# Performance work log

Hardware: AMD Instinct MI355X
Metric: run time of the kernel (lower is better)

The kernel has to match this reference:

```python
import jax, jax.numpy as jnp
import numpy as np

B, C, H, W = 4, 384, 56, 56
K, S = 5, 7


def setup_inputs() -> dict:
    key = jax.random.key(0)
    k1, k2, k3, k4, k5 = jax.random.split(key, 5)
    x = jax.random.normal(k1, (B, C, H, W), dtype=jnp.float32)
    ctx = jax.random.normal(k2, (B, C, H, W), dtype=jnp.float32)
    # 1x1 conv weights stored as (out_ch, in_ch) matrices
    Wq = jax.random.normal(k3, (C // 2, C), dtype=jnp.float32) * (1.0 / np.sqrt(C))
    Wk = jax.random.normal(k4, (C // 2, C), dtype=jnp.float32) * (1.0 / np.sqrt(C))
    Wwd = jax.random.normal(k5, (K * K, S * S), dtype=jnp.float32) * (1.0 / np.sqrt(S * S))
    return {"x": x, "ctx": ctx, "Wq": Wq, "Wk": Wk, "Wwd": Wwd}


def reference(x, ctx, Wq, Wk, Wwd):
    b, c, h, w = x.shape
    kk = K
    # q: 1x1 conv then flatten spatial -> (B, C/2, HW)
    q = jnp.einsum('dc,bchw->bdhw', Wq, x).reshape(b, c // 2, h * w)
    # adaptive avg pool to S x S (H,W multiples of S -> uniform 8x8 bins)
    ctx_p = ctx.reshape(b, c, S, h // S, S, w // S).mean(axis=(3, 5))  # (B,C,S,S)
    kf = jnp.einsum('dc,bcst->bdst', Wk, ctx_p).reshape(b, c // 2, S * S)
    # attention over region centers: (B, HW, S*S)
    A = jax.nn.softmax(jnp.einsum('bdn,bds->bns', q, kf), axis=-1)
    # dynamic per-pixel kernels via 1x1 conv S*S -> k*k: (B, k*k, H, W)
    dyn = jnp.einsum('js,bns->bjn', Wwd, A).reshape(b, kk * kk, h, w)
    # unfold x (im2col with padding k//2) -> (B, C, k*k, H, W)
    pad = kk // 2
    xp = jnp.pad(x, ((0, 0), (0, 0), (pad, pad), (pad, pad)))
    patches = jnp.stack(
        [xp[:, :, i:i + h, j:j + w] for i in range(kk) for j in range(kk)], axis=2
    )
    # per-pixel weighted reduction over the k*k taps
    out = jnp.einsum('bcjhw,bjhw->bchw', patches, dyn)
    return out
```

## Files before the change

### kernel.cpp

```cpp
#include <hip/hip_runtime.h>

#define BB 4
#define CCH 384
#define HH 56
#define WWD 56
#define HW 3136
#define S2 49
#define S2P 52
#define D2 192
#define K2 25
#define XSP 20
#define NBS 196

__global__ __launch_bounds__(256) void gtpool_k(const float* __restrict__ Wa,
                                                const float* __restrict__ Wb,
                                                const float* __restrict__ ctx,
                                                float* __restrict__ GT,
                                                float* __restrict__ PT) {
    __shared__ float sh[6144];
    int blk = blockIdx.x;
    int t = threadIdx.x;
    if (blk < 576) {
        float* As = sh;
        float* Bs = sh + 3072;
        int bi = blk % 24, bj = blk / 24;
        int tj = t & 15, ti = t >> 4;
#pragma unroll
        for (int k = 0; k < 3; k++) {
            int idx = t + 256 * k;
            int d = idx >> 2, q = idx & 3;
            *(float4*)&As[idx * 4] = *(const float4*)&Wa[(size_t)d * CCH + bi * 16 + 4 * q];
            *(float4*)&Bs[idx * 4] = *(const float4*)&Wb[(size_t)d * CCH + bj * 16 + 4 * q];
        }
        __syncthreads();
        float acc = 0.f;
#pragma unroll 8
        for (int d = 0; d < D2; d++)
            acc += As[d * 16 + ti] * Bs[d * 16 + tj];
        GT[(size_t)(bi * 16 + ti) * CCH + bj * 16 + tj] = acc;
    } else {
        float* part = sh;
        int pb = blk - 576;
        int b  = pb / 84;
        int rem = pb - b * 84;
        int sy = rem / 12;
        int cg = rem - sy * 12;
        int c0 = cg * 32;
        const float* base = ctx + ((size_t)(b * CCH + c0)) * HW + sy * 8 * WWD;
#pragma unroll
        for (int k = 0; k < 14; k++) {
            int g = t + 256 * k;
            int cc = g / 112;
            int r2 = g - cc * 112;
            float4 v = *(const float4*)(base + (size_t)cc * HW + 4 * r2);
            part[g] = (v.x + v.y) + (v.z + v.w);
        }
        __syncthreads();
        if (t < 224) {
            int cc = t / 7, sx = t - cc * 7;
            float sum = 0.f;
#pragma unroll
            for (int r = 0; r < 8; r++) {
                sum += part[cc * 112 + r * 14 + 2 * sx]
                     + part[cc * 112 + r * 14 + 2 * sx + 1];
            }
            int bs = b * S2 + sy * 7 + sx;
            PT[(size_t)(c0 + cc) * NBS + bs] = sum * (1.f / 64.f);
        }
    }
}

__global__ __launch_bounds__(256) void mv2_k(const float* __restrict__ GTt,
                                             const float* __restrict__ PT,
                                             float* __restrict__ M) {
    int t = threadIdx.x;
    int r = blockIdx.x * 2 + (t >> 7);
    int c = t & 127;
    bool has1 = (c < NBS - 128);
    int c1 = has1 ? c + 128 : c;
    const float* g = GTt + (size_t)r * CCH;
    float a0 = 0.f, a1 = 0.f;
#pragma unroll 8
    for (int i = 0; i < CCH; i++) {
        float gv = g[i];
        a0 += gv * PT[(size_t)i * NBS + c];
        a1 += gv * PT[(size_t)i * NBS + c1];
    }
    int b0 = c / S2, s0 = c - b0 * S2;
    M[((size_t)(b0 * CCH + r)) * S2P + s0] = a0;
    if (has1) {
        int bs1 = c + 128;
        int b1 = bs1 / S2, s1 = bs1 - b1 * S2;
        M[((size_t)(b1 * CCH + r)) * S2P + s1] = a1;
    }
    if (c >= 68 && c < 80) {
        int rem = c - 68;
        int bb = rem / 3, sp = 49 + rem % 3;
        M[((size_t)(bb * CCH + r)) * S2P + sp] = 0.f;
    }
}

__global__ __launch_bounds__(256) void attn_k(const float* __restrict__ x,
                                              const float* __restrict__ M,
                                              const float* __restrict__ Wwd,
                                              float* __restrict__ dyn) {
    __shared__ __align__(16) float smem[96 * XSP + 96 * S2P];
    __shared__ __align__(16) float sc[16 * S2P];
    __shared__ __align__(16) float wl[K2 * S2P];
    float* xs  = smem;
    float* Ms  = smem + 96 * XSP;
    float* red = smem;

    int b  = blockIdx.x / 196;
    int n0 = (blockIdx.x % 196) * 16;
    int t  = threadIdx.x;
    int pxg = t & 3, sg = (t >> 2) & 3, slice = t >> 4;

    float4 acc4[4][4];
#pragma unroll
    for (int k = 0; k < 4; k++)
#pragma unroll
        for (int j = 0; j < 4; j++) acc4[k][j] = make_float4(0.f, 0.f, 0.f, 0.f);

    const float* xb = x + (size_t)b * CCH * HW + n0;
    const float* Mb = M + (size_t)b * CCH * S2P;

#pragma unroll
    for (int k = 0; k < 5; k++) {
        int i = t + 256 * k;
        int j = i / S2P, ss = i - j * S2P;
        wl[i] = (ss < S2) ? Wwd[j * S2 + ss] : 0.f;
    }
    if (t < 20) {
        int i = t + 1280;
        int j = i / S2P, ss = i - j * S2P;
        wl[i] = (ss < S2) ? Wwd[j * S2 + ss] : 0.f;
    }

    int r0 = t >> 2, cq = t & 3;
    int r1 = (t + 256) >> 2;
    float4 px0, px1, pm0, pm1, pm2, pm3, pm4;

#define ATTN_LOAD(c0)                                                          \
    {                                                                          \
        px0 = *(const float4*)&xb[(size_t)((c0) + r0) * HW + 4 * cq];          \
        if (t < 128)                                                           \
            px1 = *(const float4*)&xb[(size_t)((c0) + r1) * HW + 4 * cq];      \
        const float* srcm = Mb + (size_t)(c0) * S2P;                           \
        pm0 = *(const float4*)&srcm[4 * t];                                    \
        pm1 = *(const float4*)&srcm[4 * (t + 256)];                            \
        pm2 = *(const float4*)&srcm[4 * (t + 512)];                            \
        pm3 = *(const float4*)&srcm[4 * (t + 768)];                            \
        if (t < 224) pm4 = *(const float4*)&srcm[4 * (t + 1024)];              \
    }

#define ATTN_WRITE()                                                           \
    {                                                                          \
        *(float4*)&xs[r0 * XSP + 4 * cq] = px0;                                \
        if (t < 128) *(float4*)&xs[r1 * XSP + 4 * cq] = px1;                   \
        *(float4*)&Ms[4 * t] = pm0;                                            \
        *(float4*)&Ms[4 * (t + 256)] = pm1;                                    \
        *(float4*)&Ms[4 * (t + 512)] = pm2;                                    \
        *(float4*)&Ms[4 * (t + 768)] = pm3;                                    \
        if (t < 224) *(float4*)&Ms[4 * (t + 1024)] = pm4;                      \
    }

    ATTN_LOAD(0);
    for (int ch = 0; ch < 4; ch++) {
        ATTN_WRITE();
        __syncthreads();
        if (ch < 3) { ATTN_LOAD((ch + 1) * 96); }
        int rbase = 6 * slice;
#pragma unroll
        for (int m = 0; m < 6; m++) {
            int r = rbase + m;
            const float4 xv = *(const float4*)&xs[r * XSP + 4 * pxg];
#pragma unroll
            for (int k = 0; k < 3; k++) {
                int g = sg + 4 * k;
                const float4 mv = *(const float4*)&Ms[r * S2P + 4 * g];
                acc4[k][0].x += mv.x * xv.x; acc4[k][0].y += mv.x * xv.y;
                acc4[k][0].z += mv.x * xv.z; acc4[k][0].w += mv.x * xv.w;
                acc4[k][1].x += mv.y * xv.x; acc4[k][1].y += mv.y * xv.y;
                acc4[k][1].z += mv.y * xv.z; acc4[k][1].w += mv.y * xv.w;
                acc4[k][2].x += mv.z * xv.x; acc4[k][2].y += mv.z * xv.y;
                acc4[k][2].z += mv.z * xv.z; acc4[k][2].w += mv.z * xv.w;
                acc4[k][3].x += mv.w * xv.x; acc4[k][3].y += mv.w * xv.y;
                acc4[k][3].z += mv.w * xv.z; acc4[k][3].w += mv.w * xv.w;
            }
            if (sg == 0) {
                const float4 mv = *(const float4*)&Ms[r * S2P + 48];
                acc4[3][0].x += mv.x * xv.x; acc4[3][0].y += mv.x * xv.y;
                acc4[3][0].z += mv.x * xv.z; acc4[3][0].w += mv.x * xv.w;
                acc4[3][1].x += mv.y * xv.x; acc4[3][1].y += mv.y * xv.y;
                acc4[3][1].z += mv.y * xv.z; acc4[3][1].w += mv.y * xv.w;
                acc4[3][2].x += mv.z * xv.x; acc4[3][2].y += mv.z * xv.y;
                acc4[3][2].z += mv.z * xv.z; acc4[3][2].w += mv.z * xv.w;
                acc4[3][3].x += mv.w * xv.x; acc4[3][3].y += mv.w * xv.y;
                acc4[3][3].z += mv.w * xv.z; acc4[3][3].w += mv.w * xv.w;
            }
        }
        __syncthreads();
    }

#pragma unroll
    for (int k = 0; k < 4; k++)
#pragma unroll
        for (int j = 0; j < 4; j++) {
            acc4[k][j].x += __shfl_xor(acc4[k][j].x, 16);
            acc4[k][j].y += __shfl_xor(acc4[k][j].y, 16);
            acc4[k][j].z += __shfl_xor(acc4[k][j].z, 16);
            acc4[k][j].w += __shfl_xor(acc4[k][j].w, 16);
            acc4[k][j].x += __shfl_xor(acc4[k][j].x, 32);
            acc4[k][j].y += __shfl_xor(acc4[k][j].y, 32);
            acc4[k][j].z += __shfl_xor(acc4[k][j].z, 32);
            acc4[k][j].w += __shfl_xor(acc4[k][j].w, 32);
        }

    if ((t & 63) < 16) {
        int wv = t >> 6;
        float* rb = red + (size_t)wv * 16 * S2P;
#pragma unroll
        for (int k = 0; k < 4; k++) {
            int g = sg + 4 * k;
            if (g < 13) {
                *(float4*)&rb[(4 * pxg + 0) * S2P + 4 * g] =
                    make_float4(acc4[k][0].x, acc4[k][1].x, acc4[k][2].x, acc4[k][3].x);
                *(float4*)&rb[(4 * pxg + 1) * S2P + 4 * g] =
                    make_float4(acc4[k][0].y, acc4[k][1].y, acc4[k][2].y, acc4[k][3].y);
                *(float4*)&rb[(4 * pxg + 2) * S2P + 4 * g] =
                    make_float4(acc4[k][0].z, acc4[k][1].z, acc4[k][2].z, acc4[k][3].z);
                *(float4*)&rb[(4 * pxg + 3) * S2P + 4 * g] =
                    make_float4(acc4[k][0].w, acc4[k][1].w, acc4[k][2].w, acc4[k][3].w);
            }
        }
    }
    __syncthreads();

    if (t < 208) {
        int px = t / 13, q = t - px * 13;
        float4 ssum = make_float4(0.f, 0.f, 0.f, 0.f);
#pragma unroll
        for (int wv = 0; wv < 4; wv++) {
            float4 vv = *(float4*)&red[(size_t)(wv * 16 + px) * S2P + 4 * q];
            ssum.x += vv.x; ssum.y += vv.y; ssum.z += vv.z; ssum.w += vv.w;
        }
        *(float4*)&sc[px * S2P + 4 * q] = ssum;
    }
    __syncthreads();

    if (t < 128) {
        int px = t >> 3, li = t & 7;
        float mx = -3.4e38f;
#pragma unroll
        for (int k = 0; k < 7; k++) { int s = li + 8 * k; if (s < S2) mx = fmaxf(mx, sc[px * S2P + s]); }
        mx = fmaxf(mx, __shfl_xor(mx, 1, 8));
        mx = fmaxf(mx, __shfl_xor(mx, 2, 8));
        mx = fmaxf(mx, __shfl_xor(mx, 4, 8));
        float e[7]; float sum = 0.f;
#pragma unroll
        for (int k = 0; k < 7; k++) {
            int s = li + 8 * k;
            if (s < S2) { e[k] = __expf(sc[px * S2P + s] - mx); sum += e[k]; }
        }
        sum += __shfl_xor(sum, 1, 8);
        sum += __shfl_xor(sum, 2, 8);
        sum += __shfl_xor(sum, 4, 8);
        float inv = 1.f / sum;
#pragma unroll
        for (int k = 0; k < 7; k++) {
            int s = li + 8 * k;
            if (s < S2) sc[px * S2P + s] = e[k] * inv;
        }
    }
    __syncthreads();

    float* dynb = dyn + (size_t)b * K2 * HW + n0;
#pragma unroll
    for (int pass = 0; pass < 2; pass++) {
        int o = t + 256 * pass;
        if (pass == 0 || t < 144) {
            int j = o >> 4, px = o & 15;
            float a = 0.f;
#pragma unroll
            for (int q = 0; q < 13; q++) {
                float4 wv = *(float4*)&wl[j * S2P + 4 * q];
                float4 pv = *(float4*)&sc[px * S2P + 4 * q];
                a += wv.x * pv.x + wv.y * pv.y + wv.z * pv.z + wv.w * pv.w;
            }
            dynb[(size_t)j * HW + px] = a;
        }
    }
#undef ATTN_LOAD
#undef ATTN_WRITE
}

__global__ __launch_bounds__(256, 3) void out_k(const float* __restrict__ x,
                                                const float* __restrict__ dyn,
                                                float* __restrict__ out) {
    __shared__ float xt[16][12][60];
    int blk    = blockIdx.x;
    int stripe = blk % 7;
    int cg     = (blk / 7) % 24;
    int b      = blk / (7 * 24);
    int h0 = stripe * 8;
    int c0 = cg * 16;
    int t  = threadIdx.x;
    const float* xb = x + ((size_t)(b * CCH + c0)) * HW;

    if (t < 192) {
        int cc = t / 12, r = t % 12;
        xt[cc][r][0] = 0.f; xt[cc][r][1] = 0.f;
        xt[cc][r][58] = 0.f; xt[cc][r][59] = 0.f;
    }
#pragma unroll
    for (int k = 0; k < 11; k++) {
        int idx = t + 256 * k;
        if (k < 10 || t < 128) {
            int cc  = idx / 168;
            int rem = idx - cc * 168;
            int r   = rem / 14;
            int q   = rem - r * 14;
            int h   = h0 - 2 + r;
            float4 v = make_float4(0.f, 0.f, 0.f, 0.f);
            if ((unsigned)h < (unsigned)HH)
                v = *(const float4*)&xb[(size_t)cc * HW + h * WWD + 4 * q];
            xt[cc][r][2 + 4 * q + 0] = v.x;
            xt[cc][r][2 + 4 * q + 1] = v.y;
            xt[cc][r][2 + 4 * q + 2] = v.z;
            xt[cc][r][2 + 4 * q + 3] = v.w;
        }
    }

    bool act = t < 224;
    int w = t % 56;
    int u = t / 56;
    int n = (h0 + 2 * u) * WWD + w;
    float dv0[K2], dv1[K2];
    if (act) {
        const float* db = dyn + (size_t)b * K2 * HW + n;
#pragma unroll
        for (int j = 0; j < K2; j++) {
            dv0[j] = db[(size_t)j * HW];
            dv1[j] = db[(size_t)j * HW + WWD];
        }
    }
    __syncthreads();
    if (!act) return;

    float* ob = out + ((size_t)(b * CCH + c0)) * HW + n;
#pragma unroll
    for (int cc = 0; cc < 16; cc++) {
        float a0 = 0.f, a1 = 0.f;
#pragma unroll
        for (int rr = 0; rr < 6; rr++) {
            int lr = 2 * u + rr;
            float v0 = xt[cc][lr][w + 0];
            float v1 = xt[cc][lr][w + 1];
            float v2 = xt[cc][lr][w + 2];
            float v3 = xt[cc][lr][w + 3];
            float v4 = xt[cc][lr][w + 4];
            if (rr < 5) {
                int o5 = rr * 5;
                a0 += v0 * dv0[o5] + v1 * dv0[o5 + 1] + v2 * dv0[o5 + 2]
                    + v3 * dv0[o5 + 3] + v4 * dv0[o5 + 4];
            }
            if (rr >= 1) {
                int o5 = (rr - 1) * 5;
                a1 += v0 * dv1[o5] + v1 * dv1[o5 + 1] + v2 * dv1[o5 + 2]
                    + v3 * dv1[o5 + 3] + v4 * dv1[o5 + 4];
            }
        }
        ob[(size_t)cc * HW] = a0;
        ob[(size_t)cc * HW + WWD] = a1;
    }
}

extern "C" void kernel_launch(void* const* d_in, const int* in_sizes, int n_in,
                              void* d_out, int out_size, void* d_ws, size_t ws_size,
                              hipStream_t stream) {
    const float* x   = (const float*)d_in[0];
    const float* ctx = (const float*)d_in[1];
    const float* Wq  = (const float*)d_in[2];
    const float* Wk  = (const float*)d_in[3];
    const float* Wwd = (const float*)d_in[4];
    float* out = (float*)d_out;
    float* ws  = (float*)d_ws;

    float* GT  = ws;
    float* M   = ws + 147456;
    float* dyn = ws + 147456 + 79872;
    float* PT  = dyn;

    gtpool_k<<<576 + 336, 256, 0, stream>>>(Wq, Wk, ctx, GT, PT);
    mv2_k<<<CCH / 2, 256, 0, stream>>>(GT, PT, M);
    attn_k<<<BB * 196, 256, 0, stream>>>(x, M, Wwd, dyn);
    out_k<<<BB * 24 * 7, 256, 0, stream>>>(x, dyn, out);
}
```

Baseline: 149.4 us.

## Widen attention tile to 32 pixels with 512-thread blocks

The attention-score kernel now handles 32 pixels per block with 512 threads instead of 16 pixels with 256 threads, which halves the grid. Each M tile loaded into shared memory is reused across twice as many pixels, so redundant loads of M drop. The cross-warp reduction is reorganised into two passes through shared memory, with the upper four waves adding into the lower four waves' partial sums. Fewer blocks (392) on a large GPU could reduce occupancy and parallelism, and the block now carries more shared memory and extra barriers.

```diff
diff --git a/kernel.cpp b/kernel.cpp
--- a/kernel.cpp
+++ b/kernel.cpp
@@ -9,8 +9,9 @@
 #define S2P 52
 #define D2 192
 #define K2 25
-#define XSP 20
 #define NBS 196
+#define PX 32
+#define XS2 32
 
 __global__ __launch_bounds__(256) void gtpool_k(const float* __restrict__ Wa,
                                                 const float* __restrict__ Wb,
@@ -100,21 +101,21 @@
     }
 }
 
-__global__ __launch_bounds__(256) void attn_k(const float* __restrict__ x,
-                                              const float* __restrict__ M,
-                                              const float* __restrict__ Wwd,
-                                              float* __restrict__ dyn) {
-    __shared__ __align__(16) float smem[96 * XSP + 96 * S2P];
-    __shared__ __align__(16) float sc[16 * S2P];
+__global__ __launch_bounds__(512, 4) void attn_k(const float* __restrict__ x,
+                                                 const float* __restrict__ M,
+                                                 const float* __restrict__ Wwd,
+                                                 float* __restrict__ dyn) {
+    __shared__ __align__(16) float smem[96 * XS2 + 96 * S2P];
+    __shared__ __align__(16) float sc[PX * S2P];
     __shared__ __align__(16) float wl[K2 * S2P];
     float* xs  = smem;
-    float* Ms  = smem + 96 * XSP;
+    float* Ms  = smem + 96 * XS2;
     float* red = smem;
 
-    int b  = blockIdx.x / 196;
-    int n0 = (blockIdx.x % 196) * 16;
+    int b  = blockIdx.x / 98;
+    int n0 = (blockIdx.x % 98) * PX;
     int t  = threadIdx.x;
-    int pxg = t & 3, sg = (t >> 2) & 3, slice = t >> 4;
+    int pxg = t & 7, sg = (t >> 3) & 3, slice = t >> 5;
 
     float4 acc4[4][4];
 #pragma unroll
@@ -126,43 +127,39 @@
     const float* Mb = M + (size_t)b * CCH * S2P;
 
 #pragma unroll
-    for (int k = 0; k < 5; k++) {
-        int i = t + 256 * k;
+    for (int k = 0; k < 2; k++) {
+        int i = t + 512 * k;
         int j = i / S2P, ss = i - j * S2P;
         wl[i] = (ss < S2) ? Wwd[j * S2 + ss] : 0.f;
     }
-    if (t < 20) {
-        int i = t + 1280;
+    if (t < 276) {
+        int i = t + 1024;
         int j = i / S2P, ss = i - j * S2P;
         wl[i] = (ss < S2) ? Wwd[j * S2 + ss] : 0.f;
     }
 
-    int r0 = t >> 2, cq = t & 3;
-    int r1 = (t + 256) >> 2;
-    float4 px0, px1, pm0, pm1, pm2, pm3, pm4;
+    int rx0 = t >> 3, qx = t & 7;
+    int rx1 = rx0 + 64;
+    float4 pxa, pxb, pm0, pm1, pm2;
 
 #define ATTN_LOAD(c0)                                                          \
     {                                                                          \
-        px0 = *(const float4*)&xb[(size_t)((c0) + r0) * HW + 4 * cq];          \
-        if (t < 128)                                                           \
-            px1 = *(const float4*)&xb[(size_t)((c0) + r1) * HW + 4 * cq];      \
+        pxa = *(const float4*)&xb[(size_t)((c0) + rx0) * HW + 4 * qx];         \
+        if (t < 256)                                                           \
+            pxb = *(const float4*)&xb[(size_t)((c0) + rx1) * HW + 4 * qx];     \
         const float* srcm = Mb + (size_t)(c0) * S2P;                           \
         pm0 = *(const float4*)&srcm[4 * t];                                    \
-        pm1 = *(const float4*)&srcm[4 * (t + 256)];                            \
-        pm2 = *(const float4*)&srcm[4 * (t + 512)];                            \
-        pm3 = *(const float4*)&srcm[4 * (t + 768)];                            \
-        if (t < 224) pm4 = *(const float4*)&srcm[4 * (t + 1024)];              \
+        pm1 = *(const float4*)&srcm[4 * (t + 512)];                            \
+        if (t < 224) pm2 = *(const float4*)&srcm[4 * (t + 1024)];              \
     }
 
 #define ATTN_WRITE()                                                           \
     {                                                                          \
-        *(float4*)&xs[r0 * XSP + 4 * cq] = px0;                                \
-        if (t < 128) *(float4*)&xs[r1 * XSP + 4 * cq] = px1;                   \
+        *(float4*)&xs[rx0 * XS2 + 4 * qx] = pxa;                               \
+        if (t < 256) *(float4*)&xs[rx1 * XS2 + 4 * qx] = pxb;                  \
         *(float4*)&Ms[4 * t] = pm0;                                            \
-        *(float4*)&Ms[4 * (t + 256)] = pm1;                                    \
-        *(float4*)&Ms[4 * (t + 512)] = pm2;                                    \
-        *(float4*)&Ms[4 * (t + 768)] = pm3;                                    \
-        if (t < 224) *(float4*)&Ms[4 * (t + 1024)] = pm4;                      \
+        *(float4*)&Ms[4 * (t + 512)] = pm1;                                    \
+        if (t < 224) *(float4*)&Ms[4 * (t + 1024)] = pm2;                      \
     }
 
     ATTN_LOAD(0);
@@ -174,7 +171,7 @@
 #pragma unroll
         for (int m = 0; m < 6; m++) {
             int r = rbase + m;
-            const float4 xv = *(const float4*)&xs[r * XSP + 4 * pxg];
+            const float4 xv = *(const float4*)&xs[r * XS2 + 4 * pxg];
 #pragma unroll
             for (int k = 0; k < 3; k++) {
                 int g = sg + 4 * k;
@@ -207,19 +204,15 @@
     for (int k = 0; k < 4; k++)
 #pragma unroll
         for (int j = 0; j < 4; j++) {
-            acc4[k][j].x += __shfl_xor(acc4[k][j].x, 16);
-            acc4[k][j].y += __shfl_xor(acc4[k][j].y, 16);
-            acc4[k][j].z += __shfl_xor(acc4[k][j].z, 16);
-            acc4[k][j].w += __shfl_xor(acc4[k][j].w, 16);
             acc4[k][j].x += __shfl_xor(acc4[k][j].x, 32);
             acc4[k][j].y += __shfl_xor(acc4[k][j].y, 32);
             acc4[k][j].z += __shfl_xor(acc4[k][j].z, 32);
             acc4[k][j].w += __shfl_xor(acc4[k][j].w, 32);
         }
 
-    if ((t & 63) < 16) {
-        int wv = t >> 6;
-        float* rb = red + (size_t)wv * 16 * S2P;
+    int l = t & 63, wv = t >> 6;
+    if (wv < 4 && l < 32) {
+        float* rb = red + (size_t)wv * PX * S2P;
 #pragma unroll
         for (int k = 0; k < 4; k++) {
             int g = sg + 4 * k;
@@ -236,20 +229,42 @@
         }
     }
     __syncthreads();
-
-    if (t < 208) {
+    if (wv >= 4 && l < 32) {
+        float* rb = red + (size_t)(wv - 4) * PX * S2P;
+#pragma unroll
+        for (int k = 0; k < 4; k++) {
+            int g = sg + 4 * k;
+            if (g < 13) {
+                float4 o0 = *(float4*)&rb[(4 * pxg + 0) * S2P + 4 * g];
+                float4 o1 = *(float4*)&rb[(4 * pxg + 1) * S2P + 4 * g];
+                float4 o2 = *(float4*)&rb[(4 * pxg + 2) * S2P + 4 * g];
+                float4 o3 = *(float4*)&rb[(4 * pxg + 3) * S2P + 4 * g];
+                o0.x += acc4[k][0].x; o0.y += acc4[k][1].x; o0.z += acc4[k][2].x; o0.w += acc4[k][3].x;
+                o1.x += acc4[k][0].y; o1.y += acc4[k][1].y; o1.z += acc4[k][2].y; o1.w += acc4[k][3].y;
+                o2.x += acc4[k][0].z; o2.y += acc4[k][1].z; o2.z += acc4[k][2].z; o2.w += acc4[k][3].z;
+                o3.x += acc4[k][0].w; o3.y += acc4[k][1].w; o3.z += acc4[k][2].w; o3.w += acc4[k][3].w;
+                *(float4*)&rb[(4 * pxg + 0) * S2P + 4 * g] = o0;
+                *(float4*)&rb[(4 * pxg + 1) * S2P + 4 * g] = o1;
+                *(float4*)&rb[(4 * pxg + 2) * S2P + 4 * g] = o2;
+                *(float4*)&rb[(4 * pxg + 3) * S2P + 4 * g] = o3;
+            }
+        }
+    }
+    __syncthreads();
+
+    if (t < 416) {
         int px = t / 13, q = t - px * 13;
         float4 ssum = make_float4(0.f, 0.f, 0.f, 0.f);
 #pragma unroll
-        for (int wv = 0; wv < 4; wv++) {
-            float4 vv = *(float4*)&red[(size_t)(wv * 16 + px) * S2P + 4 * q];
+        for (int w = 0; w < 4; w++) {
+            float4 vv = *(float4*)&red[(size_t)(w * PX + px) * S2P + 4 * q];
             ssum.x += vv.x; ssum.y += vv.y; ssum.z += vv.z; ssum.w += vv.w;
         }
         *(float4*)&sc[px * S2P + 4 * q] = ssum;
     }
     __syncthreads();
 
-    if (t < 128) {
+    if (t < 256) {
         int px = t >> 3, li = t & 7;
         float mx = -3.4e38f;
 #pragma unroll
@@ -278,15 +293,15 @@
     float* dynb = dyn + (size_t)b * K2 * HW + n0;
 #pragma unroll
     for (int pass = 0; pass < 2; pass++) {
-        int o = t + 256 * pass;
-        if (pass == 0 || t < 144) {
-            int j = o >> 4, px = o & 15;
+        int o = t + 512 * pass;
+        if (pass == 0 || t < 288) {
+            int j = o >> 5, px = o & 31;
             float a = 0.f;
 #pragma unroll
             for (int q = 0; q < 13; q++) {
-                float4 wv = *(float4*)&wl[j * S2P + 4 * q];
-                float4 pv = *(float4*)&sc[px * S2P + 4 * q];
-                a += wv.x * pv.x + wv.y * pv.y + wv.z * pv.z + wv.w * pv.w;
+                float4 wv4 = *(float4*)&wl[j * S2P + 4 * q];
+                float4 pv  = *(float4*)&sc[px * S2P + 4 * q];
+                a += wv4.x * pv.x + wv4.y * pv.y + wv4.z * pv.z + wv4.w * pv.w;
             }
             dynb[(size_t)j * HW + px] = a;
         }
@@ -394,6 +409,6 @@
 
     gtpool_k<<<576 + 336, 256, 0, stream>>>(Wq, Wk, ctx, GT, PT);
     mv2_k<<<CCH / 2, 256, 0, stream>>>(GT, PT, M);
-    attn_k<<<BB * 196, 256, 0, stream>>>(x, M, Wwd, dyn);
+    attn_k<<<BB * 98, 512, 0, stream>>>(x, M, Wwd, dyn);
     out_k<<<BB * 24 * 7, 256, 0, stream>>>(x, dyn, out);
 }
```

After: 342.4 us. 2.29x slower.

## Fuse four kernels into one cooperative persistent kernel with grid syncs

Applied to the files above, without the earlier changes.

Replaces the four separate launches (weight-product/pooling, matvec, attention, output) with a single cooperative kernel that walks virtual blocks in grid-stride loops and uses grid.sync between stages. The aim is to remove launch gaps and per-kernel tail effects. In exchange it adds grid-wide barriers, a larger shared-memory footprint with launch_bounds(256,2) that may lower occupancy, and a grid sized from an assumed count of 256 CUs.

```diff
diff --git a/kernel.cpp b/kernel.cpp
--- a/kernel.cpp
+++ b/kernel.cpp
@@ -1,4 +1,6 @@
 #include <hip/hip_runtime.h>
+#include <hip/hip_cooperative_groups.h>
+namespace cg = cooperative_groups;
 
 #define BB 4
 #define CCH 384
@@ -12,134 +14,128 @@
 #define XSP 20
 #define NBS 196
 
-__global__ __launch_bounds__(256) void gtpool_k(const float* __restrict__ Wa,
-                                                const float* __restrict__ Wb,
-                                                const float* __restrict__ ctx,
-                                                float* __restrict__ GT,
-                                                float* __restrict__ PT) {
-    __shared__ float sh[6144];
-    int blk = blockIdx.x;
-    int t = threadIdx.x;
-    if (blk < 576) {
-        float* As = sh;
-        float* Bs = sh + 3072;
-        int bi = blk % 24, bj = blk / 24;
-        int tj = t & 15, ti = t >> 4;
-#pragma unroll
-        for (int k = 0; k < 3; k++) {
-            int idx = t + 256 * k;
-            int d = idx >> 2, q = idx & 3;
-            *(float4*)&As[idx * 4] = *(const float4*)&Wa[(size_t)d * CCH + bi * 16 + 4 * q];
-            *(float4*)&Bs[idx * 4] = *(const float4*)&Wb[(size_t)d * CCH + bj * 16 + 4 * q];
+__global__ __launch_bounds__(256, 2) void mega_k(
+    const float* __restrict__ x, const float* __restrict__ ctx,
+    const float* __restrict__ Wq, const float* __restrict__ Wk,
+    const float* __restrict__ Wwd, float* __restrict__ GT,
+    float* __restrict__ PT, float* __restrict__ M,
+    float* __restrict__ dyn, float* __restrict__ out)
+{
+    cg::grid_group grid = cg::this_grid();
+    __shared__ float sh[11520];
+    const int bid = blockIdx.x, t = threadIdx.x, G = gridDim.x;
+
+    for (int vb = bid; vb < 912; vb += G) {
+        if (vb < 576) {
+            float* As = sh; float* Bs = sh + 3072;
+            int bi = vb % 24, bj = vb / 24;
+            int tj = t & 15, ti = t >> 4;
+#pragma unroll
+            for (int k = 0; k < 3; k++) {
+                int idx = t + 256 * k;
+                int d = idx >> 2, q = idx & 3;
+                *(float4*)&As[idx * 4] = *(const float4*)&Wq[(size_t)d * CCH + bi * 16 + 4 * q];
+                *(float4*)&Bs[idx * 4] = *(const float4*)&Wk[(size_t)d * CCH + bj * 16 + 4 * q];
+            }
+            __syncthreads();
+            float acc = 0.f;
+#pragma unroll 8
+            for (int d = 0; d < D2; d++)
+                acc += As[d * 16 + ti] * Bs[d * 16 + tj];
+            GT[(size_t)(bi * 16 + ti) * CCH + bj * 16 + tj] = acc;
+        } else {
+            float* part = sh;
+            int pb = vb - 576;
+            int b  = pb / 84;
+            int rem = pb - b * 84;
+            int sy = rem / 12;
+            int cgrp = rem - sy * 12;
+            int c0 = cgrp * 32;
+            const float* base = ctx + ((size_t)(b * CCH + c0)) * HW + sy * 8 * WWD;
+#pragma unroll
+            for (int k = 0; k < 14; k++) {
+                int g = t + 256 * k;
+                int cc = g / 112;
+                int r2 = g - cc * 112;
+                float4 v = *(const float4*)(base + (size_t)cc * HW + 4 * r2);
+                part[g] = (v.x + v.y) + (v.z + v.w);
+            }
+            __syncthreads();
+            if (t < 224) {
+                int cc = t / 7, sx = t - cc * 7;
+                float sum = 0.f;
+#pragma unroll
+                for (int r = 0; r < 8; r++)
+                    sum += part[cc * 112 + r * 14 + 2 * sx]
+                         + part[cc * 112 + r * 14 + 2 * sx + 1];
+                int bs = b * S2 + sy * 7 + sx;
+                PT[(size_t)(c0 + cc) * NBS + bs] = sum * (1.f / 64.f);
+            }
         }
         __syncthreads();
-        float acc = 0.f;
+    }
+    grid.sync();
+
+    if (bid < 192) {
+        int r = bid * 2 + (t >> 7);
+        int c = t & 127;
+        bool has1 = (c < NBS - 128);
+        int c1 = has1 ? c + 128 : c;
+        const float* g = GT + (size_t)r * CCH;
+        float a0 = 0.f, a1 = 0.f;
 #pragma unroll 8
-        for (int d = 0; d < D2; d++)
-            acc += As[d * 16 + ti] * Bs[d * 16 + tj];
-        GT[(size_t)(bi * 16 + ti) * CCH + bj * 16 + tj] = acc;
-    } else {
-        float* part = sh;
-        int pb = blk - 576;
-        int b  = pb / 84;
-        int rem = pb - b * 84;
-        int sy = rem / 12;
-        int cg = rem - sy * 12;
-        int c0 = cg * 32;
-        const float* base = ctx + ((size_t)(b * CCH + c0)) * HW + sy * 8 * WWD;
-#pragma unroll
-        for (int k = 0; k < 14; k++) {
-            int g = t + 256 * k;
-            int cc = g / 112;
-            int r2 = g - cc * 112;
-            float4 v = *(const float4*)(base + (size_t)cc * HW + 4 * r2);
-            part[g] = (v.x + v.y) + (v.z + v.w);
-        }
-        __syncthreads();
-        if (t < 224) {
-            int cc = t / 7, sx = t - cc * 7;
-            float sum = 0.f;
-#pragma unroll
-            for (int r = 0; r < 8; r++) {
-                sum += part[cc * 112 + r * 14 + 2 * sx]
-                     + part[cc * 112 + r * 14 + 2 * sx + 1];
-            }
-            int bs = b * S2 + sy * 7 + sx;
-            PT[(size_t)(c0 + cc) * NBS + bs] = sum * (1.f / 64.f);
-        }
-    }
-}
-
-__global__ __launch_bounds__(256) void mv2_k(const float* __restrict__ GTt,
-                                             const float* __restrict__ PT,
-                                             float* __restrict__ M) {
-    int t = threadIdx.x;
-    int r = blockIdx.x * 2 + (t >> 7);
-    int c = t & 127;
-    bool has1 = (c < NBS - 128);
-    int c1 = has1 ? c + 128 : c;
-    const float* g = GTt + (size_t)r * CCH;
-    float a0 = 0.f, a1 = 0.f;
-#pragma unroll 8
-    for (int i = 0; i < CCH; i++) {
-        float gv = g[i];
-        a0 += gv * PT[(size_t)i * NBS + c];
-        a1 += gv * PT[(size_t)i * NBS + c1];
-    }
-    int b0 = c / S2, s0 = c - b0 * S2;
-    M[((size_t)(b0 * CCH + r)) * S2P + s0] = a0;
-    if (has1) {
-        int bs1 = c + 128;
-        int b1 = bs1 / S2, s1 = bs1 - b1 * S2;
-        M[((size_t)(b1 * CCH + r)) * S2P + s1] = a1;
-    }
-    if (c >= 68 && c < 80) {
-        int rem = c - 68;
-        int bb = rem / 3, sp = 49 + rem % 3;
-        M[((size_t)(bb * CCH + r)) * S2P + sp] = 0.f;
-    }
-}
-
-__global__ __launch_bounds__(256) void attn_k(const float* __restrict__ x,
-                                              const float* __restrict__ M,
-                                              const float* __restrict__ Wwd,
-                                              float* __restrict__ dyn) {
-    __shared__ __align__(16) float smem[96 * XSP + 96 * S2P];
-    __shared__ __align__(16) float sc[16 * S2P];
-    __shared__ __align__(16) float wl[K2 * S2P];
-    float* xs  = smem;
-    float* Ms  = smem + 96 * XSP;
-    float* red = smem;
-
-    int b  = blockIdx.x / 196;
-    int n0 = (blockIdx.x % 196) * 16;
-    int t  = threadIdx.x;
-    int pxg = t & 3, sg = (t >> 2) & 3, slice = t >> 4;
-
-    float4 acc4[4][4];
-#pragma unroll
-    for (int k = 0; k < 4; k++)
-#pragma unroll
-        for (int j = 0; j < 4; j++) acc4[k][j] = make_float4(0.f, 0.f, 0.f, 0.f);
-
-    const float* xb = x + (size_t)b * CCH * HW + n0;
-    const float* Mb = M + (size_t)b * CCH * S2P;
-
-#pragma unroll
-    for (int k = 0; k < 5; k++) {
-        int i = t + 256 * k;
-        int j = i / S2P, ss = i - j * S2P;
-        wl[i] = (ss < S2) ? Wwd[j * S2 + ss] : 0.f;
-    }
-    if (t < 20) {
-        int i = t + 1280;
-        int j = i / S2P, ss = i - j * S2P;
-        wl[i] = (ss < S2) ? Wwd[j * S2 + ss] : 0.f;
-    }
-
-    int r0 = t >> 2, cq = t & 3;
-    int r1 = (t + 256) >> 2;
-    float4 px0, px1, pm0, pm1, pm2, pm3, pm4;
+        for (int i = 0; i < CCH; i++) {
+            float gv = g[i];
+            a0 += gv * PT[(size_t)i * NBS + c];
+            a1 += gv * PT[(size_t)i * NBS + c1];
+        }
+        int b0 = c / S2, s0 = c - b0 * S2;
+        M[((size_t)(b0 * CCH + r)) * S2P + s0] = a0;
+        if (has1) {
+            int bs1 = c + 128;
+            int b1 = bs1 / S2, s1 = bs1 - b1 * S2;
+            M[((size_t)(b1 * CCH + r)) * S2P + s1] = a1;
+        }
+        if (c >= 68 && c < 80) {
+            int rem = c - 68;
+            int bb = rem / 3, sp = 49 + rem % 3;
+            M[((size_t)(bb * CCH + r)) * S2P + sp] = 0.f;
+        }
+    }
+    grid.sync();
+
+    {
+        float* xs  = sh;
+        float* Ms  = sh + 96 * XSP;
+        float* red = sh;
+        float* sc  = sh + 6912;
+        float* wl  = sh + 7744;
+#pragma unroll
+        for (int k = 0; k < 5; k++) {
+            int i = t + 256 * k;
+            int j = i / S2P, ss = i - j * S2P;
+            wl[i] = (ss < S2) ? Wwd[j * S2 + ss] : 0.f;
+        }
+        if (t < 20) {
+            int i = t + 1280;
+            int j = i / S2P, ss = i - j * S2P;
+            wl[i] = (ss < S2) ? Wwd[j * S2 + ss] : 0.f;
+        }
+        int pxg = t & 3, sg = (t >> 2) & 3, slice = t >> 4;
+        int r0 = t >> 2, cq = t & 3;
+        int r1 = (t + 256) >> 2;
+
+        for (int tile = bid; tile < 784; tile += G) {
+            int b  = tile / 196;
+            int n0 = (tile % 196) * 16;
+            const float* xb = x + (size_t)b * CCH * HW + n0;
+            const float* Mb = M + (size_t)b * CCH * S2P;
+            float4 acc4[4][4];
+#pragma unroll
+            for (int k = 0; k < 4; k++)
+#pragma unroll
+                for (int j = 0; j < 4; j++) acc4[k][j] = make_float4(0.f, 0.f, 0.f, 0.f);
+            float4 px0, px1, pm0, pm1, pm2, pm3, pm4;
 
 #define ATTN_LOAD(c0)                                                          \
     {                                                                          \
@@ -153,7 +149,6 @@
         pm3 = *(const float4*)&srcm[4 * (t + 768)];                            \
         if (t < 224) pm4 = *(const float4*)&srcm[4 * (t + 1024)];              \
     }
-
 #define ATTN_WRITE()                                                           \
     {                                                                          \
         *(float4*)&xs[r0 * XSP + 4 * cq] = px0;                                \
@@ -165,214 +160,215 @@
         if (t < 224) *(float4*)&Ms[4 * (t + 1024)] = pm4;                      \
     }
 
-    ATTN_LOAD(0);
-    for (int ch = 0; ch < 4; ch++) {
-        ATTN_WRITE();
-        __syncthreads();
-        if (ch < 3) { ATTN_LOAD((ch + 1) * 96); }
-        int rbase = 6 * slice;
-#pragma unroll
-        for (int m = 0; m < 6; m++) {
-            int r = rbase + m;
-            const float4 xv = *(const float4*)&xs[r * XSP + 4 * pxg];
-#pragma unroll
-            for (int k = 0; k < 3; k++) {
-                int g = sg + 4 * k;
-                const float4 mv = *(const float4*)&Ms[r * S2P + 4 * g];
-                acc4[k][0].x += mv.x * xv.x; acc4[k][0].y += mv.x * xv.y;
-                acc4[k][0].z += mv.x * xv.z; acc4[k][0].w += mv.x * xv.w;
-                acc4[k][1].x += mv.y * xv.x; acc4[k][1].y += mv.y * xv.y;
-                acc4[k][1].z += mv.y * xv.z; acc4[k][1].w += mv.y * xv.w;
-                acc4[k][2].x += mv.z * xv.x; acc4[k][2].y += mv.z * xv.y;
-                acc4[k][2].z += mv.z * xv.z; acc4[k][2].w += mv.z * xv.w;
-                acc4[k][3].x += mv.w * xv.x; acc4[k][3].y += mv.w * xv.y;
-                acc4[k][3].z += mv.w * xv.z; acc4[k][3].w += mv.w * xv.w;
-            }
-            if (sg == 0) {
-                const float4 mv = *(const float4*)&Ms[r * S2P + 48];
-                acc4[3][0].x += mv.x * xv.x; acc4[3][0].y += mv.x * xv.y;
-                acc4[3][0].z += mv.x * xv.z; acc4[3][0].w += mv.x * xv.w;
-                acc4[3][1].x += mv.y * xv.x; acc4[3][1].y += mv.y * xv.y;
-                acc4[3][1].z += mv.y * xv.z; acc4[3][1].w += mv.y * xv.w;
-                acc4[3][2].x += mv.z * xv.x; acc4[3][2].y += mv.z * xv.y;
-                acc4[3][2].z += mv.z * xv.z; acc4[3][2].w += mv.z * xv.w;
-                acc4[3][3].x += mv.w * xv.x; acc4[3][3].y += mv.w * xv.y;
-                acc4[3][3].z += mv.w * xv.z; acc4[3][3].w += mv.w * xv.w;
-            }
-        }
-        __syncthreads();
-    }
-
-#pragma unroll
-    for (int k = 0; k < 4; k++)
-#pragma unroll
-        for (int j = 0; j < 4; j++) {
-            acc4[k][j].x += __shfl_xor(acc4[k][j].x, 16);
-            acc4[k][j].y += __shfl_xor(acc4[k][j].y, 16);
-            acc4[k][j].z += __shfl_xor(acc4[k][j].z, 16);
-            acc4[k][j].w += __shfl_xor(acc4[k][j].w, 16);
-            acc4[k][j].x += __shfl_xor(acc4[k][j].x, 32);
-            acc4[k][j].y += __shfl_xor(acc4[k][j].y, 32);
-            acc4[k][j].z += __shfl_xor(acc4[k][j].z, 32);
-            acc4[k][j].w += __shfl_xor(acc4[k][j].w, 32);
-        }
-
-    if ((t & 63) < 16) {
-        int wv = t >> 6;
-        float* rb = red + (size_t)wv * 16 * S2P;
-#pragma unroll
-        for (int k = 0; k < 4; k++) {
-            int g = sg + 4 * k;
-            if (g < 13) {
-                *(float4*)&rb[(4 * pxg + 0) * S2P + 4 * g] =
-                    make_float4(acc4[k][0].x, acc4[k][1].x, acc4[k][2].x, acc4[k][3].x);
-                *(float4*)&rb[(4 * pxg + 1) * S2P + 4 * g] =
-                    make_float4(acc4[k][0].y, acc4[k][1].y, acc4[k][2].y, acc4[k][3].y);
-                *(float4*)&rb[(4 * pxg + 2) * S2P + 4 * g] =
-                    make_float4(acc4[k][0].z, acc4[k][1].z, acc4[k][2].z, acc4[k][3].z);
-                *(float4*)&rb[(4 * pxg + 3) * S2P + 4 * g] =
-                    make_float4(acc4[k][0].w, acc4[k][1].w, acc4[k][2].w, acc4[k][3].w);
-            }
-        }
-    }
-    __syncthreads();
-
-    if (t < 208) {
-        int px = t / 13, q = t - px * 13;
-        float4 ssum = make_float4(0.f, 0.f, 0.f, 0.f);
-#pragma unroll
-        for (int wv = 0; wv < 4; wv++) {
-            float4 vv = *(float4*)&red[(size_t)(wv * 16 + px) * S2P + 4 * q];
-            ssum.x += vv.x; ssum.y += vv.y; ssum.z += vv.z; ssum.w += vv.w;
-        }
-        *(float4*)&sc[px * S2P + 4 * q] = ssum;
-    }
-    __syncthreads();
-
-    if (t < 128) {
-        int px = t >> 3, li = t & 7;
-        float mx = -3.4e38f;
-#pragma unroll
-        for (int k = 0; k < 7; k++) { int s = li + 8 * k; if (s < S2) mx = fmaxf(mx, sc[px * S2P + s]); }
-        mx = fmaxf(mx, __shfl_xor(mx, 1, 8));
-        mx = fmaxf(mx, __shfl_xor(mx, 2, 8));
-        mx = fmaxf(mx, __shfl_xor(mx, 4, 8));
-        float e[7]; float sum = 0.f;
-#pragma unroll
-        for (int k = 0; k < 7; k++) {
-            int s = li + 8 * k;
-            if (s < S2) { e[k] = __expf(sc[px * S2P + s] - mx); sum += e[k]; }
-        }
-        sum += __shfl_xor(sum, 1, 8);
-        sum += __shfl_xor(sum, 2, 8);
-        sum += __shfl_xor(sum, 4, 8);
-        float inv = 1.f / sum;
-#pragma unroll
-        for (int k = 0; k < 7; k++) {
-            int s = li + 8 * k;
-            if (s < S2) sc[px * S2P + s] = e[k] * inv;
-        }
-    }
-    __syncthreads();
-
-    float* dynb = dyn + (size_t)b * K2 * HW + n0;
-#pragma unroll
-    for (int pass = 0; pass < 2; pass++) {
-        int o = t + 256 * pass;
-        if (pass == 0 || t < 144) {
-            int j = o >> 4, px = o & 15;
-            float a = 0.f;
-#pragma unroll
-            for (int q = 0; q < 13; q++) {
-                float4 wv = *(float4*)&wl[j * S2P + 4 * q];
-                float4 pv = *(float4*)&sc[px * S2P + 4 * q];
-                a += wv.x * pv.x + wv.y * pv.y + wv.z * pv.z + wv.w * pv.w;
-            }
-            dynb[(size_t)j * HW + px] = a;
-        }
-    }
+            ATTN_LOAD(0);
+            for (int chn = 0; chn < 4; chn++) {
+                ATTN_WRITE();
+                __syncthreads();
+                if (chn < 3) { ATTN_LOAD((chn + 1) * 96); }
+                int rbase = 6 * slice;
+#pragma unroll
+                for (int m = 0; m < 6; m++) {
+                    int r = rbase + m;
+                    const float4 xv = *(const float4*)&xs[r * XSP + 4 * pxg];
+#pragma unroll
+                    for (int k = 0; k < 3; k++) {
+                        int g = sg + 4 * k;
+                        const float4 mv = *(const float4*)&Ms[r * S2P + 4 * g];
+                        acc4[k][0].x += mv.x * xv.x; acc4[k][0].y += mv.x * xv.y;
+                        acc4[k][0].z += mv.x * xv.z; acc4[k][0].w += mv.x * xv.w;
+                        acc4[k][1].x += mv.y * xv.x; acc4[k][1].y += mv.y * xv.y;
+                        acc4[k][1].z += mv.y * xv.z; acc4[k][1].w += mv.y * xv.w;
+                        acc4[k][2].x += mv.z * xv.x; acc4[k][2].y += mv.z * xv.y;
+                        acc4[k][2].z += mv.z * xv.z; acc4[k][2].w += mv.z * xv.w;
+                        acc4[k][3].x += mv.w * xv.x; acc4[k][3].y += mv.w * xv.y;
+                        acc4[k][3].z += mv.w * xv.z; acc4[k][3].w += mv.w * xv.w;
+                    }
+                    if (sg == 0) {
+                        const float4 mv = *(const float4*)&Ms[r * S2P + 48];
+                        acc4[3][0].x += mv.x * xv.x; acc4[3][0].y += mv.x * xv.y;
+                        acc4[3][0].z += mv.x * xv.z; acc4[3][0].w += mv.x * xv.w;
+                        acc4[3][1].x += mv.y * xv.x; acc4[3][1].y += mv.y * xv.y;
+                        acc4[3][1].z += mv.y * xv.z; acc4[3][1].w += mv.y * xv.w;
+                        acc4[3][2].x += mv.z * xv.x; acc4[3][2].y += mv.z * xv.y;
+                        acc4[3][2].z += mv.z * xv.z; acc4[3][2].w += mv.z * xv.w;
+                        acc4[3][3].x += mv.w * xv.x; acc4[3][3].y += mv.w * xv.y;
+                        acc4[3][3].z += mv.w * xv.z; acc4[3][3].w += mv.w * xv.w;
+                    }
+                }
+                __syncthreads();
+            }
 #undef ATTN_LOAD
 #undef ATTN_WRITE
-}
-
-__global__ __launch_bounds__(256, 3) void out_k(const float* __restrict__ x,
-                                                const float* __restrict__ dyn,
-                                                float* __restrict__ out) {
-    __shared__ float xt[16][12][60];
-    int blk    = blockIdx.x;
-    int stripe = blk % 7;
-    int cg     = (blk / 7) % 24;
-    int b      = blk / (7 * 24);
-    int h0 = stripe * 8;
-    int c0 = cg * 16;
-    int t  = threadIdx.x;
-    const float* xb = x + ((size_t)(b * CCH + c0)) * HW;
-
-    if (t < 192) {
-        int cc = t / 12, r = t % 12;
-        xt[cc][r][0] = 0.f; xt[cc][r][1] = 0.f;
-        xt[cc][r][58] = 0.f; xt[cc][r][59] = 0.f;
-    }
-#pragma unroll
-    for (int k = 0; k < 11; k++) {
-        int idx = t + 256 * k;
-        if (k < 10 || t < 128) {
-            int cc  = idx / 168;
-            int rem = idx - cc * 168;
-            int r   = rem / 14;
-            int q   = rem - r * 14;
-            int h   = h0 - 2 + r;
-            float4 v = make_float4(0.f, 0.f, 0.f, 0.f);
-            if ((unsigned)h < (unsigned)HH)
-                v = *(const float4*)&xb[(size_t)cc * HW + h * WWD + 4 * q];
-            xt[cc][r][2 + 4 * q + 0] = v.x;
-            xt[cc][r][2 + 4 * q + 1] = v.y;
-            xt[cc][r][2 + 4 * q + 2] = v.z;
-            xt[cc][r][2 + 4 * q + 3] = v.w;
-        }
-    }
-
-    bool act = t < 224;
-    int w = t % 56;
-    int u = t / 56;
-    int n = (h0 + 2 * u) * WWD + w;
-    float dv0[K2], dv1[K2];
-    if (act) {
-        const float* db = dyn + (size_t)b * K2 * HW + n;
-#pragma unroll
-        for (int j = 0; j < K2; j++) {
-            dv0[j] = db[(size_t)j * HW];
-            dv1[j] = db[(size_t)j * HW + WWD];
-        }
-    }
-    __syncthreads();
-    if (!act) return;
-
-    float* ob = out + ((size_t)(b * CCH + c0)) * HW + n;
-#pragma unroll
-    for (int cc = 0; cc < 16; cc++) {
-        float a0 = 0.f, a1 = 0.f;
-#pragma unroll
-        for (int rr = 0; rr < 6; rr++) {
-            int lr = 2 * u + rr;
-            float v0 = xt[cc][lr][w + 0];
-            float v1 = xt[cc][lr][w + 1];
-            float v2 = xt[cc][lr][w + 2];
-            float v3 = xt[cc][lr][w + 3];
-            float v4 = xt[cc][lr][w + 4];
-            if (rr < 5) {
-                int o5 = rr * 5;
-                a0 += v0 * dv0[o5] + v1 * dv0[o5 + 1] + v2 * dv0[o5 + 2]
-                    + v3 * dv0[o5 + 3] + v4 * dv0[o5 + 4];
-            }
-            if (rr >= 1) {
-                int o5 = (rr - 1) * 5;
-                a1 += v0 * dv1[o5] + v1 * dv1[o5 + 1] + v2 * dv1[o5 + 2]
-                    + v3 * dv1[o5 + 3] + v4 * dv1[o5 + 4];
-            }
-        }
-        ob[(size_t)cc * HW] = a0;
-        ob[(size_t)cc * HW + WWD] = a1;
+
+#pragma unroll
+            for (int k = 0; k < 4; k++)
+#pragma unroll
+                for (int j = 0; j < 4; j++) {
+                    acc4[k][j].x += __shfl_xor(acc4[k][j].x, 16);
+                    acc4[k][j].y += __shfl_xor(acc4[k][j].y, 16);
+                    acc4[k][j].z += __shfl_xor(acc4[k][j].z, 16);
+                    acc4[k][j].w += __shfl_xor(acc4[k][j].w, 16);
+                    acc4[k][j].x += __shfl_xor(acc4[k][j].x, 32);
+                    acc4[k][j].y += __shfl_xor(acc4[k][j].y, 32);
+                    acc4[k][j].z += __shfl_xor(acc4[k][j].z, 32);
+                    acc4[k][j].w += __shfl_xor(acc4[k][j].w, 32);
+                }
+
+            if ((t & 63) < 16) {
+                int wv = t >> 6;
+                float* rb = red + (size_t)wv * 16 * S2P;
+#pragma unroll
+                for (int k = 0; k < 4; k++) {
+                    int g = sg + 4 * k;
+                    if (g < 13) {
+                        *(float4*)&rb[(4 * pxg + 0) * S2P + 4 * g] =
+                            make_float4(acc4[k][0].x, acc4[k][1].x, acc4[k][2].x, acc4[k][3].x);
+                        *(float4*)&rb[(4 * pxg + 1) * S2P + 4 * g] =
+                            make_float4(acc4[k][0].y, acc4[k][1].y, acc4[k][2].y, acc4[k][3].y);
+                        *(float4*)&rb[(4 * pxg + 2) * S2P + 4 * g] =
+                            make_float4(acc4[k][0].z, acc4[k][1].z, acc4[k][2].z, acc4[k][3].z);
+                        *(float4*)&rb[(4 * pxg + 3) * S2P + 4 * g] =
+                            make_float4(acc4[k][0].w, acc4[k][1].w, acc4[k][2].w, acc4[k][3].w);
+                    }
+                }
+            }
+            __syncthreads();
+
+            if (t < 208) {
+                int px = t / 13, q = t - px * 13;
+                float4 ssum = make_float4(0.f, 0.f, 0.f, 0.f);
+#pragma unroll
+                for (int wv = 0; wv < 4; wv++) {
+                    float4 vv = *(float4*)&red[(size_t)(wv * 16 + px) * S2P + 4 * q];
+                    ssum.x += vv.x; ssum.y += vv.y; ssum.z += vv.z; ssum.w += vv.w;
+                }
+                *(float4*)&sc[px * S2P + 4 * q] = ssum;
+            }
+            __syncthreads();
+
+            if (t < 128) {
+                int px = t >> 3, li = t & 7;
+                float mx = -3.4e38f;
+#pragma unroll
+                for (int k = 0; k < 7; k++) { int s = li + 8 * k; if (s < S2) mx = fmaxf(mx, sc[px * S2P + s]); }
+                mx = fmaxf(mx, __shfl_xor(mx, 1, 8));
+                mx = fmaxf(mx, __shfl_xor(mx, 2, 8));
+                mx = fmaxf(mx, __shfl_xor(mx, 4, 8));
+                float e[7]; float sum = 0.f;
+#pragma unroll
+                for (int k = 0; k < 7; k++) {
+                    int s = li + 8 * k;
+                    if (s < S2) { e[k] = __expf(sc[px * S2P + s] - mx); sum += e[k]; }
+                }
+                sum += __shfl_xor(sum, 1, 8);
+                sum += __shfl_xor(sum, 2, 8);
+                sum += __shfl_xor(sum, 4, 8);
+                float inv = 1.f / sum;
+#pragma unroll
+                for (int k = 0; k < 7; k++) {
+                    int s = li + 8 * k;
+                    if (s < S2) sc[px * S2P + s] = e[k] * inv;
+                }
+            }
+            __syncthreads();
+
+            float* dynb = dyn + (size_t)b * K2 * HW + n0;
+#pragma unroll
+            for (int pass = 0; pass < 2; pass++) {
+                int o = t + 256 * pass;
+                if (pass == 0 || t < 144) {
+                    int j = o >> 4, px = o & 15;
+                    float a = 0.f;
+#pragma unroll
+                    for (int q = 0; q < 13; q++) {
+                        float4 wv4 = *(float4*)&wl[j * S2P + 4 * q];
+                        float4 pv  = *(float4*)&sc[px * S2P + 4 * q];
+                        a += wv4.x * pv.x + wv4.y * pv.y + wv4.z * pv.z + wv4.w * pv.w;
+                    }
+                    dynb[(size_t)j * HW + px] = a;
+                }
+            }
+            __syncthreads();
+        }
+    }
+    grid.sync();
+
+    for (int vb = bid; vb < 672; vb += G) {
+        float (*xt)[12][60] = (float (*)[12][60])sh;
+        int stripe = vb % 7;
+        int cgrp   = (vb / 7) % 24;
+        int b      = vb / (7 * 24);
+        int h0 = stripe * 8;
+        int c0 = cgrp * 16;
+        const float* xb = x + ((size_t)(b * CCH + c0)) * HW;
+
+        if (t < 192) {
+            int cc = t / 12, r = t % 12;
+            xt[cc][r][0] = 0.f; xt[cc][r][1] = 0.f;
+            xt[cc][r][58] = 0.f; xt[cc][r][59] = 0.f;
+        }
+#pragma unroll
+        for (int k = 0; k < 11; k++) {
+            int idx = t + 256 * k;
+            if (k < 10 || t < 128) {
+                int cc  = idx / 168;
+                int rem = idx - cc * 168;
+                int r   = rem / 14;
+                int q   = rem - r * 14;
+                int h   = h0 - 2 + r;
+                float4 v = make_float4(0.f, 0.f, 0.f, 0.f);
+                if ((unsigned)h < (unsigned)HH)
+                    v = *(const float4*)&xb[(size_t)cc * HW + h * WWD + 4 * q];
+                xt[cc][r][2 + 4 * q + 0] = v.x;
+                xt[cc][r][2 + 4 * q + 1] = v.y;
+                xt[cc][r][2 + 4 * q + 2] = v.z;
+                xt[cc][r][2 + 4 * q + 3] = v.w;
+            }
+        }
+
+        bool act = t < 224;
+        int w = t % 56;
+        int u = t / 56;
+        int n = (h0 + 2 * u) * WWD + w;
+        float dv0[K2], dv1[K2];
+        if (act) {
+            const float* db = dyn + (size_t)b * K2 * HW + n;
+#pragma unroll
+            for (int j = 0; j < K2; j++) {
+                dv0[j] = db[(size_t)j * HW];
+                dv1[j] = db[(size_t)j * HW + WWD];
+            }
+        }
+        __syncthreads();
+        if (act) {
+            float* ob = out + ((size_t)(b * CCH + c0)) * HW + n;
+#pragma unroll
+            for (int cc = 0; cc < 16; cc++) {
+                float a0 = 0.f, a1 = 0.f;
+#pragma unroll
+                for (int rr = 0; rr < 6; rr++) {
+                    int lr = 2 * u + rr;
+                    float v0 = xt[cc][lr][w + 0];
+                    float v1 = xt[cc][lr][w + 1];
+                    float v2 = xt[cc][lr][w + 2];
+                    float v3 = xt[cc][lr][w + 3];
+                    float v4 = xt[cc][lr][w + 4];
+                    if (rr < 5) {
+                        int o5 = rr * 5;
+                        a0 += v0 * dv0[o5] + v1 * dv0[o5 + 1] + v2 * dv0[o5 + 2]
+                            + v3 * dv0[o5 + 3] + v4 * dv0[o5 + 4];
+                    }
+                    if (rr >= 1) {
+                        int o5 = (rr - 1) * 5;
+                        a1 += v0 * dv1[o5] + v1 * dv1[o5 + 1] + v2 * dv1[o5 + 2]
+                            + v3 * dv1[o5 + 3] + v4 * dv1[o5 + 4];
+                    }
+                }
+                ob[(size_t)cc * HW] = a0;
+                ob[(size_t)cc * HW + WWD] = a1;
+            }
+        }
+        __syncthreads();
     }
 }
 
@@ -392,8 +388,17 @@
     float* dyn = ws + 147456 + 79872;
     float* PT  = dyn;
 
-    gtpool_k<<<576 + 336, 256, 0, stream>>>(Wq, Wk, ctx, GT, PT);
-    mv2_k<<<CCH / 2, 256, 0, stream>>>(GT, PT, M);
-    attn_k<<<BB * 196, 256, 0, stream>>>(x, M, Wwd, dyn);
-    out_k<<<BB * 24 * 7, 256, 0, stream>>>(x, dyn, out);
+    static int maxb = 0;
+    if (maxb == 0) {
+        hipOccupancyMaxActiveBlocksPerMultiprocessor(
+            &maxb, reinterpret_cast<const void*>(mega_k), 256, 0);
+        if (maxb < 1) maxb = 1;
+    }
+    int gridn = maxb * 256;
+    if (gridn > 912) gridn = 912;
+
+    void* args[] = {(void*)&x, (void*)&ctx, (void*)&Wq, (void*)&Wk, (void*)&Wwd,
+                    (void*)&GT, (void*)&PT, (void*)&M, (void*)&dyn, (void*)&out};
+    hipLaunchCooperativeKernel(reinterpret_cast<const void*>(mega_k),
+                               dim3(gridn), dim3(256), args, 0, stream);
 }
```

Measured after the change: 274.7 us. 1.84x slower.
